# Kernel tuning notes

Measured on AMD Instinct MI355X. Metric: run time of the kernel, lower is better.

## Reference

```python
import jax, jax.numpy as jnp
import numpy as np

B, T, C, H = 2, 2048, 1024, 16
D = C // H  # head_dim = 64

def setup_inputs() -> dict:
    key = jax.random.key(0)
    k0, k1, k2, k3, k4 = jax.random.split(key, 5)
    s = 1.0 / np.sqrt(C)
    return {
        "x": jax.random.normal(k0, (B, T, C), dtype=jnp.float32),
        "w_qkv": jax.random.uniform(k1, (C, 3 * C), jnp.float32, -s, s),
        "b_qkv": jax.random.uniform(k2, (3 * C,), jnp.float32, -s, s),
        "w_proj": jax.random.uniform(k3, (C, C), jnp.float32, -s, s),
        "b_proj": jax.random.uniform(k4, (C,), jnp.float32, -s, s),
    }

def reference(x, w_qkv, b_qkv, w_proj, b_proj):
    Bx, Tx, Cx = x.shape
    qkv = x @ w_qkv + b_qkv                      # [B,T,3C]
    q, k, v = jnp.split(qkv, 3, axis=-1)
    # [B,T,C] -> [B,H,T,D]
    def heads(t):
        return t.reshape(Bx, Tx, H, D).transpose(0, 2, 1, 3)
    q, k, v = heads(q), heads(k), heads(v)
    att = jnp.einsum('bhqd,bhkd->bhqk', q, k) / np.sqrt(D).astype(np.float32)
    causal = jnp.tril(jnp.ones((Tx, Tx), dtype=bool))
    att = jnp.where(causal, att, -jnp.inf)
    att = jax.nn.softmax(att, axis=-1)
    y = jnp.einsum('bhqk,bhkd->bhqd', att, v)    # [B,H,T,D]
    y = y.transpose(0, 2, 1, 3).reshape(Bx, Tx, Cx)
    return y @ w_proj + b_proj
```

## Files before the change

### kernel.cpp

```cpp
#include <hip/hip_runtime.h>

typedef short bf16x8 __attribute__((ext_vector_type(8)));
typedef float f32x4 __attribute__((ext_vector_type(4)));
typedef unsigned short u16;
typedef unsigned short u16x8 __attribute__((ext_vector_type(8)));
typedef float f32x4_a __attribute__((ext_vector_type(4), may_alias));

__device__ __forceinline__ u16 f2bf(float f) {
    union { float f; unsigned u; } v; v.f = f;
    unsigned r = v.u + 0x7fffu + ((v.u >> 16) & 1u);
    return (u16)(r >> 16);
}
__device__ __forceinline__ u16 f2bf_rhu(float f) {
    union { float f; unsigned u; } v; v.f = f;
    return (u16)((v.u + 0x8000u) >> 16);
}

__device__ __forceinline__ void gld_lds16(const void* g, void* l) {
    __builtin_amdgcn_global_load_lds(
        (const __attribute__((address_space(1))) void*)g,
        (__attribute__((address_space(3))) void*)l, 16, 0, 0);
}

__global__ __launch_bounds__(256) void prep_kernel(
    const float* __restrict__ x, u16* __restrict__ xb,
    const float* __restrict__ w_qkv, u16* __restrict__ wqkvT) {
    __shared__ float tile[32][33];
    const int b = blockIdx.x, tid = threadIdx.x;
    if (b < 2048) {
        const int i = b * 256 + tid;
        float4 a = ((const float4*)x)[i * 2];
        float4 c = ((const float4*)x)[i * 2 + 1];
        u16x8 h;
        h[0] = f2bf(a.x); h[1] = f2bf(a.y); h[2] = f2bf(a.z); h[3] = f2bf(a.w);
        h[4] = f2bf(c.x); h[5] = f2bf(c.y); h[6] = f2bf(c.z); h[7] = f2bf(c.w);
        *(u16x8*)(xb + (size_t)i * 8) = h;
        return;
    }
    const int bx = b - 2048;
    const int n0 = (bx % 96) * 32, k0 = (bx / 96) * 32;
    const int tx = tid & 31, ty = tid >> 5;
#pragma unroll
    for (int i = 0; i < 32; i += 8)
        tile[ty + i][tx] = w_qkv[(size_t)(k0 + ty + i) * 3072 + n0 + tx];
    __syncthreads();
#pragma unroll
    for (int i = 0; i < 32; i += 8)
        wqkvT[(size_t)(n0 + ty + i) * 1024 + k0 + tx] = f2bf(tile[tx][ty + i]);
}

#define QSCALE 0.180336880f

template <int OUTMODE, int BN>
__global__ __launch_bounds__(256) void gemm_m97(
    const u16* __restrict__ A, const u16* __restrict__ Bt,
    const float* __restrict__ bias, float* __restrict__ Cf,
    u16* __restrict__ Qo, u16* __restrict__ Ko, u16* __restrict__ Vt,
    int M, int N, int K) {
    constexpr int NF = BN / 32;
    __shared__ __align__(16) u16 lA[128 * 64];
    __shared__ __align__(16) u16 lB[BN * 64];

    const int tid = threadIdx.x;
    const int lane = tid & 63, wid = tid >> 6;
    const int wr = wid >> 1, wc = wid & 1;
    const int fr = lane & 15, fq = lane >> 4;
    const int m0 = blockIdx.y * 128, n0 = blockIdx.x * BN;

    const int gsrc = (lane & 7) ^ (lane >> 3);
    const u16* gA0 = A + (size_t)(m0 + (tid >> 3)) * K + gsrc * 8;
    const u16* gB0 = Bt + (size_t)(n0 + (tid >> 3)) * K + gsrc * 8;
    u16* lAw = lA + wid * 512;
    u16* lBw = lB + wid * 512;

    const int r7 = fr & 7;
    const int gk[2] = { ((0 + fq) ^ r7) * 8, ((4 + fq) ^ r7) * 8 };

    f32x4 acc[4][NF];
#pragma unroll
    for (int m = 0; m < 4; m++)
#pragma unroll
        for (int n = 0; n < NF; n++)
#pragma unroll
            for (int r = 0; r < 4; r++) acc[m][n][r] = 0.f;

    for (int k0 = 0; k0 < K; k0 += 64) {
        __syncthreads();
#pragma unroll
        for (int c = 0; c < 4; c++)
            gld_lds16(gA0 + (size_t)(c * 32) * K + k0, lAw + c * 2048);
#pragma unroll
        for (int c = 0; c < BN / 32; c++)
            gld_lds16(gB0 + (size_t)(c * 32) * K + k0, lBw + c * 2048);
        __syncthreads();

#pragma unroll
        for (int kf = 0; kf < 2; kf++) {
            bf16x8 a[4], b[NF];
#pragma unroll
            for (int m = 0; m < 4; m++)
                a[m] = *(const bf16x8*)&lA[(wr * 64 + m * 16 + fr) * 64 + gk[kf]];
#pragma unroll
            for (int n = 0; n < NF; n++)
                b[n] = *(const bf16x8*)&lB[(wc * (BN / 2) + n * 16 + fr) * 64 + gk[kf]];
#pragma unroll
            for (int m = 0; m < 4; m++)
#pragma unroll
                for (int n = 0; n < NF; n++)
                    acc[m][n] = __builtin_amdgcn_mfma_f32_16x16x32_bf16(a[m], b[n], acc[m][n], 0, 0, 0);
        }
    }

#pragma unroll
    for (int m = 0; m < 4; m++) {
#pragma unroll
        for (int n = 0; n < NF; n++) {
            const int row0 = m0 + wr * 64 + m * 16 + fq * 4;
            const int col = n0 + wc * (BN / 2) + n * 16 + fr;
            float v4[4];
#pragma unroll
            for (int r = 0; r < 4; r++) v4[r] = acc[m][n][r] + bias[col];
            if (OUTMODE == 0) {
                const int bb = row0 >> 11, t0 = row0 & 2047;
                const int sec = col >> 10, cc = col & 1023;
                const int h = cc >> 6, d = cc & 63;
                if (sec == 0) {
#pragma unroll
                    for (int r = 0; r < 4; r++)
                        Qo[(((size_t)(bb * 16 + h) * 2048 + t0 + r) << 6) + d] = f2bf(v4[r] * QSCALE);
                } else if (sec == 1) {
#pragma unroll
                    for (int r = 0; r < 4; r++)
                        Ko[(((size_t)(bb * 16 + h) * 2048 + t0 + r) << 6) + d] = f2bf(v4[r]);
                } else {
                    ushort4 p;
                    p.x = f2bf(v4[0]); p.y = f2bf(v4[1]); p.z = f2bf(v4[2]); p.w = f2bf(v4[3]);
                    *(ushort4*)&Vt[(((size_t)(bb * 16 + h) * 64 + d) << 11) + t0] = p;
                }
            } else {
#pragma unroll
                for (int r = 0; r < 4; r++)
                    Cf[(size_t)(row0 + r) * N + col] = v4[r];
            }
        }
    }
}

__global__ __launch_bounds__(256, 4) void attn_kernel(const u16* __restrict__ Q,
                                                      const u16* __restrict__ Kg,
                                                      const u16* __restrict__ Vt,
                                                      u16* __restrict__ O,
                                                      const float* __restrict__ wp,
                                                      u16* __restrict__ wpT) {
    __shared__ __align__(16) u16 smem[12288];

    const int tid = threadIdx.x;

    if (blockIdx.x >= 1024) {
        float* tile = (float*)smem;
        const int bx = blockIdx.x - 1024;
        const int n0 = (bx & 31) * 32, k0 = (bx >> 5) * 32;
        const int tx = tid & 31, ty = tid >> 5;
#pragma unroll
        for (int i = 0; i < 32; i += 8)
            tile[(ty + i) * 33 + tx] = wp[(size_t)(k0 + ty + i) * 1024 + n0 + tx];
        __syncthreads();
#pragma unroll
        for (int i = 0; i < 32; i += 8)
            wpT[(size_t)(n0 + ty + i) * 1024 + k0 + tx] = f2bf(tile[tx * 33 + ty + i]);
        return;
    }

    u16* lV = smem + 8192;
    const int lane = tid & 63, wid = tid >> 6;
    const int fr = lane & 15, fq = lane >> 4;
    const int kw = wid >> 1, qw = wid & 1;
    const int bh = blockIdx.x & 31;
    const int qi = 31 - (blockIdx.x >> 5);
    const int qb0 = qi * 64;
    const size_t base = (size_t)bh * (2048 * 64);
    const u16* Qp = Q + base;
    const u16* Kp = Kg + base;
    const u16* Vp = Vt + base;

    const int q0w = qb0 + qw * 32;
    bf16x8 qa[2][2];
#pragma unroll
    for (int qg = 0; qg < 2; qg++)
#pragma unroll
        for (int kf = 0; kf < 2; kf++)
            qa[qg][kf] = *(const bf16x8*)&Qp[(size_t)(q0w + qg * 16 + fr) * 64 + kf * 32 + fq * 8];

    bf16x8 vones;
#pragma unroll
    for (int j = 0; j < 8; j++) vones[j] = (short)0x3F80;

    f32x4 o[4][2], lsum[2];
#pragma unroll
    for (int qg = 0; qg < 2; qg++) {
#pragma unroll
        for (int r = 0; r < 4; r++) lsum[qg][r] = 0.f;
#pragma unroll
        for (int dg = 0; dg < 4; dg++)
#pragma unroll
            for (int r = 0; r < 4; r++) o[dg][qg][r] = 0.f;
    }

    const int srow0 = wid * 8 + (lane >> 3);
    const int gsrc = (lane & 7) ^ (lane >> 3);
    const u16* kSrc0 = Kp + (size_t)srow0 * 64 + gsrc * 8;
    const u16* vSrc0 = Vp + ((size_t)srow0 << 11) + gsrc * 8;

    const int r7 = fr & 7;
    const int gk0 = ((0 + fq) ^ r7) * 8;
    const int gk1 = ((4 + fq) ^ r7) * 8;
    const int gkv = ((kw * 4 + fq) ^ r7) * 8;

    const int nt = qi + 1;

#define STAGE_K(bufofs, kt0_)                                                   \
    do {                                                                        \
        u16* _lkw = smem + (bufofs) + wid * 512;                                \
        gld_lds16(kSrc0 + (size_t)(kt0_) * 64, _lkw);                           \
        gld_lds16(kSrc0 + (size_t)((kt0_) + 32) * 64, _lkw + 2048);             \
    } while (0)
#define STAGE_V(kt0_)                                                           \
    do {                                                                        \
        u16* _lvw = lV + wid * 512;                                             \
        gld_lds16(vSrc0 + (kt0_), _lvw);                                        \
        gld_lds16(vSrc0 + ((size_t)32 << 11) + (kt0_), _lvw + 2048);            \
    } while (0)

    STAGE_K(0, 0);
    STAGE_V(0);
    asm volatile("s_waitcnt vmcnt(0)" ::: "memory");
    __builtin_amdgcn_s_barrier();

    for (int kt = 0; kt < nt; kt++) {
        const int kt0 = kt << 6;
        const int curofs = (kt & 1) ? 4096 : 0;

        if (kt + 1 < nt) {
            STAGE_K(curofs ^ 4096, kt0 + 64);
            asm volatile("s_waitcnt vmcnt(2)" ::: "memory");
            __builtin_amdgcn_s_barrier();
        } else if (nt > 1) {
            asm volatile("s_waitcnt vmcnt(0)" ::: "memory");
            __builtin_amdgcn_s_barrier();
        }
        const u16* lKc = smem + curofs;

        f32x4 s[2][2];
#pragma unroll
        for (int kg = 0; kg < 2; kg++)
#pragma unroll
            for (int qg = 0; qg < 2; qg++)
#pragma unroll
                for (int r = 0; r < 4; r++) s[kg][qg][r] = 0.f;
        __builtin_amdgcn_s_setprio(1);
#pragma unroll
        for (int kg = 0; kg < 2; kg++) {
            const int krow = (kw * 32 + kg * 16 + fr) * 64;
            bf16x8 kb0 = *(const bf16x8*)&lKc[krow + gk0];
            bf16x8 kb1 = *(const bf16x8*)&lKc[krow + gk1];
#pragma unroll
            for (int qg = 0; qg < 2; qg++) {
                s[kg][qg] = __builtin_amdgcn_mfma_f32_16x16x32_bf16(kb0, qa[qg][0], s[kg][qg], 0, 0, 0);
                s[kg][qg] = __builtin_amdgcn_mfma_f32_16x16x32_bf16(kb1, qa[qg][1], s[kg][qg], 0, 0, 0);
            }
        }
        __builtin_amdgcn_s_setprio(0);

        if (kt == nt - 1) {
#pragma unroll
            for (int kg = 0; kg < 2; kg++) {
                const int kg0 = kt0 + kw * 32 + kg * 16 + fq * 4;
#pragma unroll
                for (int qg = 0; qg < 2; qg++) {
                    const int qg0 = q0w + qg * 16 + fr;
#pragma unroll
                    for (int r = 0; r < 4; r++)
                        if (kg0 + r > qg0) s[kg][qg][r] = -200.f;
                }
            }
        }

        bf16x8 va[4];
#pragma unroll
        for (int dg = 0; dg < 4; dg++)
            va[dg] = *(const bf16x8*)&lV[(dg * 16 + fr) * 64 + gkv];

#pragma unroll
        for (int qg = 0; qg < 2; qg++) {
            unsigned pa = (unsigned)f2bf_rhu(__builtin_amdgcn_exp2f(s[0][qg][0])) |
                          ((unsigned)f2bf_rhu(__builtin_amdgcn_exp2f(s[0][qg][1])) << 16);
            unsigned pb_ = (unsigned)f2bf_rhu(__builtin_amdgcn_exp2f(s[0][qg][2])) |
                           ((unsigned)f2bf_rhu(__builtin_amdgcn_exp2f(s[0][qg][3])) << 16);
            unsigned pc = (unsigned)f2bf_rhu(__builtin_amdgcn_exp2f(s[1][qg][0])) |
                          ((unsigned)f2bf_rhu(__builtin_amdgcn_exp2f(s[1][qg][1])) << 16);
            unsigned pd = (unsigned)f2bf_rhu(__builtin_amdgcn_exp2f(s[1][qg][2])) |
                          ((unsigned)f2bf_rhu(__builtin_amdgcn_exp2f(s[1][qg][3])) << 16);
            asm("v_permlane32_swap_b32 %0, %1" : "+v"(pa), "+v"(pc));
            asm("v_permlane16_swap_b32 %0, %1" : "+v"(pa), "+v"(pc));
            asm("v_permlane32_swap_b32 %0, %1" : "+v"(pb_), "+v"(pd));
            asm("v_permlane16_swap_b32 %0, %1" : "+v"(pb_), "+v"(pd));
            union { unsigned u[4]; bf16x8 v; } pbu;
            pbu.u[0] = pa; pbu.u[1] = pb_; pbu.u[2] = pc; pbu.u[3] = pd;
            const bf16x8 pb = pbu.v;

            __builtin_amdgcn_s_setprio(1);
            lsum[qg] = __builtin_amdgcn_mfma_f32_16x16x32_bf16(vones, pb, lsum[qg], 0, 0, 0);
#pragma unroll
            for (int dg = 0; dg < 4; dg++)
                o[dg][qg] = __builtin_amdgcn_mfma_f32_16x16x32_bf16(va[dg], pb, o[dg][qg], 0, 0, 0);
            __builtin_amdgcn_s_setprio(0);
        }

        if (kt + 1 < nt) {
            __builtin_amdgcn_s_barrier();
            STAGE_V(kt0 + 64);
        }
    }
#undef STAGE_K
#undef STAGE_V

    __syncthreads();

    float* cmb = (float*)smem;
    float* slab = cmb + (size_t)qw * 2560 + lane * 40;
    if (kw == 1) {
#pragma unroll
        for (int dg = 0; dg < 4; dg++)
#pragma unroll
            for (int qg = 0; qg < 2; qg++)
                *(f32x4_a*)&slab[(dg * 2 + qg) * 4] = o[dg][qg];
#pragma unroll
        for (int qg = 0; qg < 2; qg++)
            *(f32x4_a*)&slab[32 + qg * 4] = lsum[qg];
    }
    __syncthreads();
    if (kw == 0) {
#pragma unroll
        for (int dg = 0; dg < 4; dg++)
#pragma unroll
            for (int qg = 0; qg < 2; qg++) {
                f32x4_a p = *(const f32x4_a*)&slab[(dg * 2 + qg) * 4];
#pragma unroll
                for (int r = 0; r < 4; r++) o[dg][qg][r] += p[r];
            }
#pragma unroll
        for (int qg = 0; qg < 2; qg++) {
            f32x4_a p = *(const f32x4_a*)&slab[32 + qg * 4];
            lsum[qg][0] += p[0];
        }

        const int bb = bh >> 4, hh = bh & 15;
#pragma unroll
        for (int qg = 0; qg < 2; qg++) {
            const float inv = 1.f / lsum[qg][0];
            u16* orow = O + ((size_t)(bb * 2048 + q0w + qg * 16 + fr)) * 1024 + hh * 64 + fq * 4;
#pragma unroll
            for (int dg = 0; dg < 4; dg++) {
                ushort4 h;
                h.x = f2bf(o[dg][qg][0] * inv);
                h.y = f2bf(o[dg][qg][1] * inv);
                h.z = f2bf(o[dg][qg][2] * inv);
                h.w = f2bf(o[dg][qg][3] * inv);
                *(ushort4*)&orow[dg * 16] = h;
            }
        }
    }
}

extern "C" void kernel_launch(void* const* d_in, const int* in_sizes, int n_in,
                              void* d_out, int out_size, void* d_ws, size_t ws_size,
                              hipStream_t stream) {
    const float* x      = (const float*)d_in[0];
    const float* w_qkv  = (const float*)d_in[1];
    const float* b_qkv  = (const float*)d_in[2];
    const float* w_proj = (const float*)d_in[3];
    const float* b_proj = (const float*)d_in[4];
    float* out = (float*)d_out;

    u16* ws = (u16*)d_ws;
    u16* wqkvT  = ws;
    u16* wprojT = wqkvT + 3072 * 1024;
    u16* Qb     = wprojT + 1024 * 1024;
    u16* Kb     = Qb + 32 * 2048 * 64;
    u16* Vtb    = Kb + 32 * 2048 * 64;
    u16* xb     = Vtb + 32 * 2048 * 64;
    u16* attnO  = xb;

    prep_kernel<<<5120, 256, 0, stream>>>(x, xb, w_qkv, wqkvT);

    gemm_m97<0, 128><<<dim3(24, 32), 256, 0, stream>>>(
        xb, wqkvT, b_qkv, nullptr, Qb, Kb, Vtb, 4096, 3072, 1024);

    attn_kernel<<<2048, 256, 0, stream>>>(Qb, Kb, Vtb, attnO, w_proj, wprojT);

    gemm_m97<1, 64><<<dim3(16, 32), 256, 0, stream>>>(
        attnO, wprojT, b_proj, out, nullptr, nullptr, nullptr, 4096, 1024, 1024);
}
```

Baseline: 94.31 us.

## Replace QKV GEMM with 256x192-tile 8-wave kernel using phased MFMA scheduling

Adds a dedicated QKV projection GEMM with 512-thread blocks and a 256x192 output tile. It double-buffers A/B in LDS through global_load_lds and splits each K-step into four barrier-separated MFMA phases with s_setprio. The larger tile raises data reuse per LDS load and cuts the grid to 256 blocks, one wave of work on the device. The cost is higher register pressure (24 accumulators per wave) and one more barrier per phase. The output GEMM is simplified to write fp32 only.

```diff
diff --git a/kernel.cpp b/kernel.cpp
--- a/kernel.cpp
+++ b/kernel.cpp
@@ -51,11 +51,162 @@
 
 #define QSCALE 0.180336880f
 
-template <int OUTMODE, int BN>
+__global__ __launch_bounds__(512, 2) void gemm_8ph(
+    const u16* __restrict__ A, const u16* __restrict__ Bt,
+    const float* __restrict__ bias,
+    u16* __restrict__ Qo, u16* __restrict__ Ko, u16* __restrict__ Vt) {
+    const int K = 1024;
+    __shared__ __align__(16) u16 smem[57344];
+
+    const int tid = threadIdx.x;
+    const int lane = tid & 63, wid = tid >> 6;
+    const int wm = wid >> 2, wn = wid & 3;
+    const int fr = lane & 15, fq = lane >> 4;
+    const int m0 = blockIdx.y * 256, n0 = blockIdx.x * 192;
+
+    const int gsrc = (tid & 7) ^ ((tid >> 3) & 7);
+    const u16* gA0 = A + (size_t)(m0 + (tid >> 3)) * K + gsrc * 8;
+    const u16* gB0 = Bt + (size_t)(n0 + (tid >> 3)) * K + gsrc * 8;
+
+    const int r7 = fr & 7;
+    const int gk0 = ((0 + fq) ^ r7) * 8;
+    const int gk1 = ((4 + fq) ^ r7) * 8;
+
+    f32x4 acc[8][3];
+#pragma unroll
+    for (int m = 0; m < 8; m++)
+#pragma unroll
+        for (int n = 0; n < 3; n++)
+#pragma unroll
+            for (int r = 0; r < 4; r++) acc[m][n][r] = 0.f;
+
+#define STAGE8(t)                                                               \
+    do {                                                                        \
+        const int _b = (t) & 1;                                                 \
+        const size_t _ko = (size_t)(t) * 64;                                    \
+        u16* _la = smem + _b * 16384 + wid * 512;                               \
+        u16* _lb = smem + 32768 + _b * 12288 + wid * 512;                       \
+        gld_lds16(gA0 + _ko, _la);                                              \
+        gld_lds16(gA0 + (size_t)64 * 1024 + _ko, _la + 4096);                   \
+        gld_lds16(gA0 + (size_t)128 * 1024 + _ko, _la + 8192);                  \
+        gld_lds16(gA0 + (size_t)192 * 1024 + _ko, _la + 12288);                 \
+        gld_lds16(gB0 + _ko, _lb);                                              \
+        gld_lds16(gB0 + (size_t)64 * 1024 + _ko, _lb + 4096);                   \
+        gld_lds16(gB0 + (size_t)128 * 1024 + _ko, _lb + 8192);                  \
+    } while (0)
+
+    STAGE8(0);
+    asm volatile("s_waitcnt vmcnt(0)" ::: "memory");
+    __builtin_amdgcn_s_barrier();
+
+    for (int t = 0; t < 16; t++) {
+        const int b = t & 1;
+        const u16* lA = smem + b * 16384;
+        const u16* lB = smem + 32768 + b * 12288;
+        if (t + 1 < 16) STAGE8(t + 1);
+
+        bf16x8 aR[4][2], b01[2][2], b2[2];
+
+#pragma unroll
+        for (int mf = 0; mf < 4; mf++) {
+            const int row = (wm * 128 + mf * 16 + fr) * 64;
+            aR[mf][0] = *(const bf16x8*)&lA[row + gk0];
+            aR[mf][1] = *(const bf16x8*)&lA[row + gk1];
+        }
+#pragma unroll
+        for (int nf = 0; nf < 2; nf++) {
+            const int row = (wn * 48 + nf * 16 + fr) * 64;
+            b01[nf][0] = *(const bf16x8*)&lB[row + gk0];
+            b01[nf][1] = *(const bf16x8*)&lB[row + gk1];
+        }
+        __builtin_amdgcn_s_setprio(1);
+#pragma unroll
+        for (int mf = 0; mf < 4; mf++)
+#pragma unroll
+            for (int nf = 0; nf < 2; nf++) {
+                acc[mf][nf] = __builtin_amdgcn_mfma_f32_16x16x32_bf16(aR[mf][0], b01[nf][0], acc[mf][nf], 0, 0, 0);
+                acc[mf][nf] = __builtin_amdgcn_mfma_f32_16x16x32_bf16(aR[mf][1], b01[nf][1], acc[mf][nf], 0, 0, 0);
+            }
+        __builtin_amdgcn_s_setprio(0);
+        __builtin_amdgcn_s_barrier();
+
+        {
+            const int row = (wn * 48 + 32 + fr) * 64;
+            b2[0] = *(const bf16x8*)&lB[row + gk0];
+            b2[1] = *(const bf16x8*)&lB[row + gk1];
+        }
+        __builtin_amdgcn_s_setprio(1);
+#pragma unroll
+        for (int mf = 0; mf < 4; mf++) {
+            acc[mf][2] = __builtin_amdgcn_mfma_f32_16x16x32_bf16(aR[mf][0], b2[0], acc[mf][2], 0, 0, 0);
+            acc[mf][2] = __builtin_amdgcn_mfma_f32_16x16x32_bf16(aR[mf][1], b2[1], acc[mf][2], 0, 0, 0);
+        }
+        __builtin_amdgcn_s_setprio(0);
+        __builtin_amdgcn_s_barrier();
+
+#pragma unroll
+        for (int mf = 0; mf < 4; mf++) {
+            const int row = (wm * 128 + 64 + mf * 16 + fr) * 64;
+            aR[mf][0] = *(const bf16x8*)&lA[row + gk0];
+            aR[mf][1] = *(const bf16x8*)&lA[row + gk1];
+        }
+        __builtin_amdgcn_s_setprio(1);
+#pragma unroll
+        for (int mf = 0; mf < 4; mf++) {
+            acc[4 + mf][2] = __builtin_amdgcn_mfma_f32_16x16x32_bf16(aR[mf][0], b2[0], acc[4 + mf][2], 0, 0, 0);
+            acc[4 + mf][2] = __builtin_amdgcn_mfma_f32_16x16x32_bf16(aR[mf][1], b2[1], acc[4 + mf][2], 0, 0, 0);
+        }
+        __builtin_amdgcn_s_setprio(0);
+        __builtin_amdgcn_s_barrier();
+
+        __builtin_amdgcn_s_setprio(1);
+#pragma unroll
+        for (int mf = 0; mf < 4; mf++)
+#pragma unroll
+            for (int nf = 0; nf < 2; nf++) {
+                acc[4 + mf][nf] = __builtin_amdgcn_mfma_f32_16x16x32_bf16(aR[mf][0], b01[nf][0], acc[4 + mf][nf], 0, 0, 0);
+                acc[4 + mf][nf] = __builtin_amdgcn_mfma_f32_16x16x32_bf16(aR[mf][1], b01[nf][1], acc[4 + mf][nf], 0, 0, 0);
+            }
+        __builtin_amdgcn_s_setprio(0);
+
+        asm volatile("s_waitcnt vmcnt(0)" ::: "memory");
+        __builtin_amdgcn_s_barrier();
+    }
+#undef STAGE8
+
+#pragma unroll
+    for (int mf = 0; mf < 8; mf++) {
+#pragma unroll
+        for (int nf = 0; nf < 3; nf++) {
+            const int row0 = m0 + wm * 128 + mf * 16 + fq * 4;
+            const int col = n0 + wn * 48 + nf * 16 + fr;
+            float v4[4];
+#pragma unroll
+            for (int r = 0; r < 4; r++) v4[r] = acc[mf][nf][r] + bias[col];
+            const int bb = row0 >> 11, t0 = row0 & 2047;
+            const int sec = col >> 10, cc = col & 1023;
+            const int h = cc >> 6, d = cc & 63;
+            if (sec == 0) {
+#pragma unroll
+                for (int r = 0; r < 4; r++)
+                    Qo[(((size_t)(bb * 16 + h) * 2048 + t0 + r) << 6) + d] = f2bf(v4[r] * QSCALE);
+            } else if (sec == 1) {
+#pragma unroll
+                for (int r = 0; r < 4; r++)
+                    Ko[(((size_t)(bb * 16 + h) * 2048 + t0 + r) << 6) + d] = f2bf(v4[r]);
+            } else {
+                ushort4 p;
+                p.x = f2bf(v4[0]); p.y = f2bf(v4[1]); p.z = f2bf(v4[2]); p.w = f2bf(v4[3]);
+                *(ushort4*)&Vt[(((size_t)(bb * 16 + h) * 64 + d) << 11) + t0] = p;
+            }
+        }
+    }
+}
+
+template <int BN>
 __global__ __launch_bounds__(256) void gemm_m97(
     const u16* __restrict__ A, const u16* __restrict__ Bt,
     const float* __restrict__ bias, float* __restrict__ Cf,
-    u16* __restrict__ Qo, u16* __restrict__ Ko, u16* __restrict__ Vt,
     int M, int N, int K) {
     constexpr int NF = BN / 32;
     __shared__ __align__(16) u16 lA[128 * 64];
@@ -117,31 +268,9 @@
         for (int n = 0; n < NF; n++) {
             const int row0 = m0 + wr * 64 + m * 16 + fq * 4;
             const int col = n0 + wc * (BN / 2) + n * 16 + fr;
-            float v4[4];
-#pragma unroll
-            for (int r = 0; r < 4; r++) v4[r] = acc[m][n][r] + bias[col];
-            if (OUTMODE == 0) {
-                const int bb = row0 >> 11, t0 = row0 & 2047;
-                const int sec = col >> 10, cc = col & 1023;
-                const int h = cc >> 6, d = cc & 63;
-                if (sec == 0) {
-#pragma unroll
-                    for (int r = 0; r < 4; r++)
-                        Qo[(((size_t)(bb * 16 + h) * 2048 + t0 + r) << 6) + d] = f2bf(v4[r] * QSCALE);
-                } else if (sec == 1) {
-#pragma unroll
-                    for (int r = 0; r < 4; r++)
-                        Ko[(((size_t)(bb * 16 + h) * 2048 + t0 + r) << 6) + d] = f2bf(v4[r]);
-                } else {
-                    ushort4 p;
-                    p.x = f2bf(v4[0]); p.y = f2bf(v4[1]); p.z = f2bf(v4[2]); p.w = f2bf(v4[3]);
-                    *(ushort4*)&Vt[(((size_t)(bb * 16 + h) * 64 + d) << 11) + t0] = p;
-                }
-            } else {
-#pragma unroll
-                for (int r = 0; r < 4; r++)
-                    Cf[(size_t)(row0 + r) * N + col] = v4[r];
-            }
+#pragma unroll
+            for (int r = 0; r < 4; r++)
+                Cf[(size_t)(row0 + r) * N + col] = acc[m][n][r] + bias[col];
         }
     }
 }
@@ -393,11 +522,10 @@
 
     prep_kernel<<<5120, 256, 0, stream>>>(x, xb, w_qkv, wqkvT);
 
-    gemm_m97<0, 128><<<dim3(24, 32), 256, 0, stream>>>(
-        xb, wqkvT, b_qkv, nullptr, Qb, Kb, Vtb, 4096, 3072, 1024);
+    gemm_8ph<<<dim3(16, 16), 512, 0, stream>>>(xb, wqkvT, b_qkv, Qb, Kb, Vtb);
 
     attn_kernel<<<2048, 256, 0, stream>>>(Qb, Kb, Vtb, attnO, w_proj, wprojT);
 
-    gemm_m97<1, 64><<<dim3(16, 32), 256, 0, stream>>>(
-        attnO, wprojT, b_proj, out, nullptr, nullptr, nullptr, 4096, 1024, 1024);
-}
+    gemm_m97<64><<<dim3(16, 32), 256, 0, stream>>>(
+        attnO, wprojT, b_proj, out, 4096, 1024, 1024);
+}
```

Result: faster. 91.68 us (-2.8%).
